# Kernel optimization log

Measured on AMD Instinct MI355X. Metric: run time of the kernel, lower is better.

The kernel has to match this reference:

```python
import jax, jax.numpy as jnp
import numpy as np

T, B, H = 32, 262144, 16  # time steps, n_learner_params (batch), hidden/feature size


def setup_inputs() -> dict:
    key = jax.random.key(0)
    ks = jax.random.split(key, 5)
    return {
        "x": jax.random.normal(ks[0], (T, B, H), dtype=jnp.float32),
        "grads": jax.random.normal(ks[1], (T, B, 1), dtype=jnp.float32),
        "WF": jax.random.uniform(ks[2], (H + 2, 1), dtype=jnp.float32, minval=-0.01, maxval=0.01),
        "WI": jax.random.uniform(ks[3], (H + 2, 1), dtype=jnp.float32, minval=-0.01, maxval=0.01),
        "cI": jax.random.uniform(ks[4], (B, 1), dtype=jnp.float32, minval=-0.01, maxval=0.01),
        "bI": jnp.zeros((1, 1), jnp.float32),
        "bF": jnp.zeros((1, 1), jnp.float32),
        "m": jnp.zeros((1,), jnp.float32),
    }


def reference(x, grads, WF, WI, cI, bI, bF, m):
    # x: [T, B, H] meta-learner inputs; grads: [T, B, 1] learner gradients.
    batch = x.shape[1]
    zeros = jnp.zeros((batch, 1), x.dtype)
    init = (zeros, zeros, cI, zeros)  # (fS, iS, cS, deltaS)

    def step(carry, inp):
        fS, iS, cS, dS = carry
        x_t, g_t = inp  # [B, H], [B, 1]
        f_new = jnp.concatenate([x_t, cS, fS], axis=1) @ WF + bF  # [B, 1]
        i_new = jnp.concatenate([x_t, cS, iS], axis=1) @ WI + bI  # [B, 1]
        d_new = m * dS - jax.nn.sigmoid(i_new) * g_t
        c_new = jax.nn.sigmoid(f_new) * cS + d_new
        return (f_new, i_new, c_new, d_new), None

    (fS, iS, cS, dS), _ = jax.lax.scan(step, init, (x, grads))
    # num_layers == 1; original stacks fS twice (repo quirk) -> shapes:
    # fS_n: [1, 1, B, 1]; iS_n/cS_n/deltaS_n: [1, B, 1]
    return (fS[None, None], iS[None], cS[None], dS[None])
```

## Files before the change

kernel.cpp:

```cpp
#include <hip/hip_runtime.h>


__device__ __forceinline__ float sigmoidf_(float v) {
    return 1.0f / (1.0f + __expf(-v));
}

__global__ __launch_bounds__(256) void metalstm_kernel(
    const float* __restrict__ x,
    const float* __restrict__ grads,
    const float* __restrict__ WF,
    const float* __restrict__ WI,
    const float* __restrict__ cI,
    const float* __restrict__ bI,
    const float* __restrict__ bF,
    const float* __restrict__ mp,
    float* __restrict__ out,
    int B, int T)
{
    int b = blockIdx.x * blockDim.x + threadIdx.x;
    if (b >= B) return;

    float wf[18], wi[18];
#pragma unroll
    for (int k = 0; k < 18; ++k) { wf[k] = WF[k]; wi[k] = WI[k]; }
    const float bf = bF[0];
    const float bi = bI[0];
    const float m  = mp[0];

    float fS = 0.0f, iS = 0.0f, cS = cI[b], dS = 0.0f;

    const float4* __restrict__ xv = reinterpret_cast<const float4*>(x);
    const size_t xbase   = (size_t)b * 4;
    const size_t xstride = (size_t)B * 4;

#pragma unroll 4
    for (int t = 0; t < T; ++t) {
        const float4* xp = xv + xbase + (size_t)t * xstride;
        float4 a0 = xp[0];
        float4 a1 = xp[1];
        float4 a2 = xp[2];
        float4 a3 = xp[3];
        float gt = grads[(size_t)t * B + b];

        float df = a0.x * wf[0];
        df = fmaf(a0.y, wf[1],  df);
        df = fmaf(a0.z, wf[2],  df);
        df = fmaf(a0.w, wf[3],  df);
        df = fmaf(a1.x, wf[4],  df);
        df = fmaf(a1.y, wf[5],  df);
        df = fmaf(a1.z, wf[6],  df);
        df = fmaf(a1.w, wf[7],  df);
        df = fmaf(a2.x, wf[8],  df);
        df = fmaf(a2.y, wf[9],  df);
        df = fmaf(a2.z, wf[10], df);
        df = fmaf(a2.w, wf[11], df);
        df = fmaf(a3.x, wf[12], df);
        df = fmaf(a3.y, wf[13], df);
        df = fmaf(a3.z, wf[14], df);
        df = fmaf(a3.w, wf[15], df);

        float di = a0.x * wi[0];
        di = fmaf(a0.y, wi[1],  di);
        di = fmaf(a0.z, wi[2],  di);
        di = fmaf(a0.w, wi[3],  di);
        di = fmaf(a1.x, wi[4],  di);
        di = fmaf(a1.y, wi[5],  di);
        di = fmaf(a1.z, wi[6],  di);
        di = fmaf(a1.w, wi[7],  di);
        di = fmaf(a2.x, wi[8],  di);
        di = fmaf(a2.y, wi[9],  di);
        di = fmaf(a2.z, wi[10], di);
        di = fmaf(a2.w, wi[11], di);
        di = fmaf(a3.x, wi[12], di);
        di = fmaf(a3.y, wi[13], di);
        di = fmaf(a3.z, wi[14], di);
        di = fmaf(a3.w, wi[15], di);

        float f_new = fmaf(cS, wf[16], fmaf(fS, wf[17], df + bf));
        float i_new = fmaf(cS, wi[16], fmaf(iS, wi[17], di + bi));
        float d_new = fmaf(m, dS, -sigmoidf_(i_new) * gt);
        float c_new = fmaf(sigmoidf_(f_new), cS, d_new);

        fS = f_new; iS = i_new; cS = c_new; dS = d_new;
    }

    out[b]             = fS;
    out[(size_t)B + b] = iS;
    out[2*(size_t)B + b] = cS;
    out[3*(size_t)B + b] = dS;
}

extern "C" void kernel_launch(void* const* d_in, const int* in_sizes, int n_in,
                              void* d_out, int out_size, void* d_ws, size_t ws_size,
                              hipStream_t stream) {
    const float* x     = (const float*)d_in[0];
    const float* grads = (const float*)d_in[1];
    const float* WF    = (const float*)d_in[2];
    const float* WI    = (const float*)d_in[3];
    const float* cI    = (const float*)d_in[4];
    const float* bI    = (const float*)d_in[5];
    const float* bF    = (const float*)d_in[6];
    const float* m     = (const float*)d_in[7];
    float* out = (float*)d_out;

    const int T = 32;
    const int B = in_sizes[4];

    dim3 block(256);
    dim3 grid((B + 255) / 256);
    metalstm_kernel<<<grid, block, 0, stream>>>(x, grads, WF, WI, cI, bI, bF, m,
                                                out, B, T);
}
```

Baseline: 105.5 us.

## Split each batch row across four lanes with shuffle reduction and nontemporal loads

Each batch element is now handled by four threads, each loading one 16-byte chunk of the 16-float feature row and computing a partial dot product, combined via xor shuffles. This makes every load instruction fully contiguous across the wavefront and quadruples the threads in flight to hide memory latency; the loads are marked nontemporal to avoid polluting caches. In exchange, the recurrent scalar math and the grads load are duplicated across the four lanes, and shuffles are added per step.

```diff
diff --git a/kernel.cpp b/kernel.cpp
--- a/kernel.cpp
+++ b/kernel.cpp
@@ -1,5 +1,7 @@
 #include <hip/hip_runtime.h>
 
+
+typedef float f32x4 __attribute__((ext_vector_type(4)));
 
 __device__ __forceinline__ float sigmoidf_(float v) {
     return 1.0f / (1.0f + __expf(-v));
@@ -17,77 +19,59 @@
     float* __restrict__ out,
     int B, int T)
 {
-    int b = blockIdx.x * blockDim.x + threadIdx.x;
+    const int tid = blockIdx.x * blockDim.x + threadIdx.x;
+    const int b   = tid >> 2;
+    const int q   = tid & 3;
     if (b >= B) return;
 
-    float wf[18], wi[18];
-#pragma unroll
-    for (int k = 0; k < 18; ++k) { wf[k] = WF[k]; wi[k] = WI[k]; }
+    const f32x4 wfv = reinterpret_cast<const f32x4*>(WF)[q];
+    const f32x4 wiv = reinterpret_cast<const f32x4*>(WI)[q];
+    const float wf16 = WF[16], wf17 = WF[17];
+    const float wi16 = WI[16], wi17 = WI[17];
     const float bf = bF[0];
     const float bi = bI[0];
     const float m  = mp[0];
 
     float fS = 0.0f, iS = 0.0f, cS = cI[b], dS = 0.0f;
 
-    const float4* __restrict__ xv = reinterpret_cast<const float4*>(x);
-    const size_t xbase   = (size_t)b * 4;
+    const f32x4* __restrict__ xv = reinterpret_cast<const f32x4*>(x);
+    const size_t xoff    = (size_t)b * 4 + q;
     const size_t xstride = (size_t)B * 4;
 
-#pragma unroll 4
+#pragma unroll 8
     for (int t = 0; t < T; ++t) {
-        const float4* xp = xv + xbase + (size_t)t * xstride;
-        float4 a0 = xp[0];
-        float4 a1 = xp[1];
-        float4 a2 = xp[2];
-        float4 a3 = xp[3];
-        float gt = grads[(size_t)t * B + b];
+        f32x4 a = __builtin_nontemporal_load(xv + xoff + (size_t)t * xstride);
+        float gt = __builtin_nontemporal_load(grads + (size_t)t * B + b);
 
-        float df = a0.x * wf[0];
-        df = fmaf(a0.y, wf[1],  df);
-        df = fmaf(a0.z, wf[2],  df);
-        df = fmaf(a0.w, wf[3],  df);
-        df = fmaf(a1.x, wf[4],  df);
-        df = fmaf(a1.y, wf[5],  df);
-        df = fmaf(a1.z, wf[6],  df);
-        df = fmaf(a1.w, wf[7],  df);
-        df = fmaf(a2.x, wf[8],  df);
-        df = fmaf(a2.y, wf[9],  df);
-        df = fmaf(a2.z, wf[10], df);
-        df = fmaf(a2.w, wf[11], df);
-        df = fmaf(a3.x, wf[12], df);
-        df = fmaf(a3.y, wf[13], df);
-        df = fmaf(a3.z, wf[14], df);
-        df = fmaf(a3.w, wf[15], df);
+        float df = a.x * wfv.x;
+        df = fmaf(a.y, wfv.y, df);
+        df = fmaf(a.z, wfv.z, df);
+        df = fmaf(a.w, wfv.w, df);
 
-        float di = a0.x * wi[0];
-        di = fmaf(a0.y, wi[1],  di);
-        di = fmaf(a0.z, wi[2],  di);
-        di = fmaf(a0.w, wi[3],  di);
-        di = fmaf(a1.x, wi[4],  di);
-        di = fmaf(a1.y, wi[5],  di);
-        di = fmaf(a1.z, wi[6],  di);
-        di = fmaf(a1.w, wi[7],  di);
-        di = fmaf(a2.x, wi[8],  di);
-        di = fmaf(a2.y, wi[9],  di);
-        di = fmaf(a2.z, wi[10], di);
-        di = fmaf(a2.w, wi[11], di);
-        di = fmaf(a3.x, wi[12], di);
-        di = fmaf(a3.y, wi[13], di);
-        di = fmaf(a3.z, wi[14], di);
-        di = fmaf(a3.w, wi[15], di);
+        float di = a.x * wiv.x;
+        di = fmaf(a.y, wiv.y, di);
+        di = fmaf(a.z, wiv.z, di);
+        di = fmaf(a.w, wiv.w, di);
 
-        float f_new = fmaf(cS, wf[16], fmaf(fS, wf[17], df + bf));
-        float i_new = fmaf(cS, wi[16], fmaf(iS, wi[17], di + bi));
+        df += __shfl_xor(df, 1, 4);
+        df += __shfl_xor(df, 2, 4);
+        di += __shfl_xor(di, 1, 4);
+        di += __shfl_xor(di, 2, 4);
+
+        float f_new = fmaf(cS, wf16, fmaf(fS, wf17, df + bf));
+        float i_new = fmaf(cS, wi16, fmaf(iS, wi17, di + bi));
         float d_new = fmaf(m, dS, -sigmoidf_(i_new) * gt);
         float c_new = fmaf(sigmoidf_(f_new), cS, d_new);
 
         fS = f_new; iS = i_new; cS = c_new; dS = d_new;
     }
 
-    out[b]             = fS;
-    out[(size_t)B + b] = iS;
-    out[2*(size_t)B + b] = cS;
-    out[3*(size_t)B + b] = dS;
+    if (q == 0) {
+        out[b]               = fS;
+        out[(size_t)B + b]   = iS;
+        out[2*(size_t)B + b] = cS;
+        out[3*(size_t)B + b] = dS;
+    }
 }
 
 extern "C" void kernel_launch(void* const* d_in, const int* in_sizes, int n_in,
@@ -106,8 +90,9 @@
     const int T = 32;
     const int B = in_sizes[4];
 
+    const int nthreads = B * 4;
     dim3 block(256);
-    dim3 grid((B + 255) / 256);
+    dim3 grid((nthreads + 255) / 256);
     metalstm_kernel<<<grid, block, 0, stream>>>(x, grads, WF, WI, cI, bI, bF, m,
                                                 out, B, T);
 }
```

Result: faster. 94.99 us (-10.0%).
